# Performance work log

Measured on AMD Instinct MI355X. Metric: run time of the kernel, lower is better.

The kernel has to match this reference:

```python
import jax, jax.numpy as jnp
import numpy as np

ROI = 268
K = 32
SLOPE = 0.33
EPS = 1e-5

def leaky(h):
    return jnp.where(h >= 0, h, SLOPE * h)

def bn(h, g, b):
    # BatchNorm in training mode: biased batch statistics over the node/batch axis
    mu = h.mean(0)
    var = ((h - mu) ** 2).mean(0)
    return (h - mu) * jax.lax.rsqrt(var + EPS) * g + b


def setup_inputs():
    B, F, C, deg = 64, ROI, 32, 32
    N = B * ROI
    key = jax.random.key(0)
    ks = jax.random.split(key, 32)
    x = jax.random.normal(ks[0], (N, F), jnp.float32)
    # static within-graph edges: every node has exactly `deg` incoming edges
    tgt = jnp.repeat(jnp.arange(N, dtype=jnp.int32), deg)
    src = (tgt // ROI) * ROI + jax.random.randint(ks[1], (N * deg,), 0, ROI, dtype=jnp.int32)
    edge_index = jnp.stack([src, tgt])
    batch = jnp.repeat(jnp.arange(B, dtype=jnp.int32), ROI)
    def lin(k, i, o):
        return 0.05 * jax.random.normal(k, (i, o), jnp.float32)
    def vec(k, o):
        return 0.05 * jax.random.normal(k, (o,), jnp.float32)
    p = dict(
        x=x, edge_index=edge_index, batch=batch,
        W1a=lin(ks[2], 2 * F, C), b1a=vec(ks[3], C), W1b=lin(ks[4], C, C), b1b=vec(ks[5], C),
        g1=1.0 + vec(ks[6], C), be1=vec(ks[7], C),
        W2a=lin(ks[8], 2 * F, C), b2a=vec(ks[9], C), W2b=lin(ks[10], C, C), b2b=vec(ks[11], C),
        g2=1.0 + vec(ks[12], C), be2=vec(ks[13], C),
        W3=lin(ks[14], 2 * F, 1), b3=vec(ks[15], 1), g3=1.0 + vec(ks[16], 1), be3=vec(ks[17], 1),
        Wl1=lin(ks[18], ROI + 2 * C, 256), bl1=vec(ks[19], 256), g4=1.0 + vec(ks[20], 256), be4=vec(ks[21], 256),
        Wl2=lin(ks[22], 256, 128), bl2=vec(ks[23], 128), g5=1.0 + vec(ks[24], 128), be5=vec(ks[25], 128),
        Wl3=lin(ks[26], 128, 1), bl3=vec(ks[27], 1),
    )
    return p


def reference(x, edge_index, batch,
              W1a, b1a, W1b, b1b, g1, be1,
              W2a, b2a, W2b, b2b, g2, be2,
              W3, b3, g3, be3,
              Wl1, bl1, g4, be4, Wl2, bl2, g5, be5, Wl3, bl3):
    N, F = x.shape
    B = N // ROI
    src, tgt = edge_index[0], edge_index[1]
    xi = x[tgt]                       # [E, F] central node feature
    xd = x[src] - xi                  # [E, F] x_j - x_i
    # --- gcn1: EdgeConv(mlp1) + BN + LeakyReLU (dropout = identity in eval) ---
    m1 = leaky(xi @ W1a[:F] + xd @ W1a[F:] + b1a) @ W1b + b1b   # [E, C]
    a1 = jax.ops.segment_max(m1, tgt, num_segments=N)
    a1 = jnp.where(jnp.isfinite(a1), a1, 0.0)
    x1 = leaky(bn(a1, g1, be1))
    # --- gcn3: EdgeConv(mlp3) + BN + LeakyReLU ---
    m3 = xi @ W3[:F] + xd @ W3[F:] + b3                          # [E, 1]
    a3 = jax.ops.segment_max(m3, tgt, num_segments=N)
    a3 = jnp.where(jnp.isfinite(a3), a3, 0.0)
    x3 = leaky(bn(a3, g3, be3))
    # --- gcn2: DynamicEdgeConv(mlp2, k=32) + BN + LeakyReLU ---
    xg = x.reshape(B, ROI, F)
    sq = jnp.sum(xg * xg, -1)
    d2 = sq[:, :, None] + sq[:, None, :] - 2.0 * jnp.einsum('bif,bjf->bij', xg, xg)
    _, idx = jax.lax.top_k(-d2, K)                               # [B, ROI, K], includes self
    xj = jax.vmap(lambda f, i: f[i])(xg, idx)                    # [B, ROI, K, F]
    part_i = jnp.einsum('bif,fc->bic', xg, W2a[:F])
    part_d = jnp.einsum('bikf,fc->bikc', xj - xg[:, :, None, :], W2a[F:])
    h2 = leaky(part_i[:, :, None, :] + part_d + b2a)
    m2 = h2 @ W2b + b2b                                          # [B, ROI, K, C]
    x2 = leaky(bn(m2.max(axis=2).reshape(N, -1), g2, be2))
    # --- readout ---
    counts = jax.ops.segment_sum(jnp.ones((N, 1), x.dtype), batch, num_segments=B)
    p1 = jax.ops.segment_sum(x1, batch, num_segments=B) / counts
    p2 = jax.ops.segment_sum(x2, batch, num_segments=B) / counts
    z = jnp.concatenate([p1, p2, x3.reshape(B, ROI)], -1)        # [B, 268+64]
    z = leaky(bn(z @ Wl1 + bl1, g4, be4))
    z = leaky(bn(z @ Wl2 + bl2, g5, be5))
    return z @ Wl3 + bl3                                          # [B, 1]
```

## Files before the change

kernel.cpp:

```cpp
#include <hip/hip_runtime.h>
#include <hip/hip_bf16.h>

#define ROI   268
#define FDIM  268
#define NB    64
#define NN    (NB*ROI)
#define CC    32
#define DEG   32
#define KSEL  32
#define SLOPE 0.33f
#define EPSBN 1e-5f

typedef __attribute__((ext_vector_type(8)))  short bf16x8;
typedef __attribute__((ext_vector_type(4)))  float f32x4;
typedef __attribute__((ext_vector_type(16))) float f32x16;

__device__ __forceinline__ float lrelu(float h) { return h >= 0.f ? h : SLOPE * h; }

__device__ __forceinline__ unsigned short f2bf(float f) {
    union { __hip_bfloat16 h; unsigned short s; } u;
    u.h = __float2bfloat16(f);
    return u.s;
}
__device__ __forceinline__ float bf2f(unsigned short h) {
    return __uint_as_float(((unsigned int)h) << 16);
}

#define PREP_PACK_BLOCKS  2448
#define PREP_PACKW_BLOCKS 18
#define PREP_SCAL_BLOCKS  1072

__global__ __launch_bounds__(256) void k_prep(
    const float* __restrict__ x,
    const float* __restrict__ W1a, const float* __restrict__ W2a,
    const float* __restrict__ W3,  const float* __restrict__ b3,
    unsigned short* __restrict__ Xh, unsigned short* __restrict__ Xl,
    unsigned short* __restrict__ Wfh, unsigned short* __restrict__ Wfl,
    float* __restrict__ u3, float* __restrict__ v3, float* __restrict__ sqv)
{
    const int bid = blockIdx.x;
    const int tid = threadIdx.x;
    if (bid < PREP_PACK_BLOCKS) {
        const int gid = bid * 256 + tid;
        const int l   = gid & 63;
        const int f3  = gid >> 6;
        const int ks  = f3 % 9;
        const int bc  = f3 / 9;
        const int ct  = bc % 17;
        const int b   = bc / 17;
        const int node = ct * 16 + (l & 15);
        const int k0   = ks * 32 + (l >> 4) * 8;
        float f[8];
        #pragma unroll
        for (int j = 0; j < 8; ++j) f[j] = 0.f;
        if (node < ROI) {
            const float* row = &x[((size_t)b * ROI + node) * FDIM];
            if (k0 + 3 < FDIM) { float4 v = *(const float4*)&row[k0];     f[0]=v.x; f[1]=v.y; f[2]=v.z; f[3]=v.w; }
            if (k0 + 7 < FDIM) { float4 v = *(const float4*)&row[k0 + 4]; f[4]=v.x; f[5]=v.y; f[6]=v.z; f[7]=v.w; }
        }
        unsigned short hh[8], ll[8];
        #pragma unroll
        for (int j = 0; j < 8; ++j) {
            hh[j] = f2bf(f[j]);
            ll[j] = f2bf(f[j] - bf2f(hh[j]));
        }
        uint4 hp, lp;
        hp.x = (unsigned)hh[0] | ((unsigned)hh[1] << 16); hp.y = (unsigned)hh[2] | ((unsigned)hh[3] << 16);
        hp.z = (unsigned)hh[4] | ((unsigned)hh[5] << 16); hp.w = (unsigned)hh[6] | ((unsigned)hh[7] << 16);
        lp.x = (unsigned)ll[0] | ((unsigned)ll[1] << 16); lp.y = (unsigned)ll[2] | ((unsigned)ll[3] << 16);
        lp.z = (unsigned)ll[4] | ((unsigned)ll[5] << 16); lp.w = (unsigned)ll[6] | ((unsigned)ll[7] << 16);
        const size_t base = (size_t)f3 * 512 + l * 8;
        *(uint4*)&Xh[base] = hp;
        *(uint4*)&Xl[base] = lp;
    } else if (bid < PREP_PACK_BLOCKS + PREP_PACKW_BLOCKS) {
        const int gid = (bid - PREP_PACK_BLOCKS) * 256 + tid;
        const int l  = gid & 63;
        const int f3 = gid >> 6;
        const int ks = f3 % 9;
        const int mc = f3 / 9;
        const int ct = mc & 1;
        const int m  = mc >> 1;
        const int k0 = ks * 32 + (l >> 4) * 8;
        const int c  = ct * 16 + (l & 15);
        const float* W = (m < 2) ? W1a : W2a;
        const bool isU = (m & 1) == 0;
        unsigned short hh[8], ll[8];
        #pragma unroll
        for (int j = 0; j < 8; ++j) {
            const int kk = k0 + j;
            float val = 0.f;
            if (kk < FDIM) {
                float wb = W[(size_t)(FDIM + kk) * CC + c];
                val = isU ? (W[(size_t)kk * CC + c] - wb) : wb;
            }
            hh[j] = f2bf(val);
            ll[j] = f2bf(val - bf2f(hh[j]));
        }
        uint4 hp, lp;
        hp.x = (unsigned)hh[0] | ((unsigned)hh[1] << 16); hp.y = (unsigned)hh[2] | ((unsigned)hh[3] << 16);
        hp.z = (unsigned)hh[4] | ((unsigned)hh[5] << 16); hp.w = (unsigned)hh[6] | ((unsigned)hh[7] << 16);
        lp.x = (unsigned)ll[0] | ((unsigned)ll[1] << 16); lp.y = (unsigned)ll[2] | ((unsigned)ll[3] << 16);
        lp.z = (unsigned)ll[4] | ((unsigned)ll[5] << 16); lp.w = (unsigned)ll[6] | ((unsigned)ll[7] << 16);
        const size_t base = (size_t)f3 * 512 + l * 8;
        *(uint4*)&Wfh[base] = hp;
        *(uint4*)&Wfl[base] = lp;
    } else {
        const int s = bid - (PREP_PACK_BLOCKS + PREP_PACKW_BLOCKS);
        const int l = tid & 63;
        #pragma unroll
        for (int i = 0; i < 4; ++i) {
            const int n = s * 16 + i * 4 + (tid >> 6);
            const float* row = &x[(size_t)n * FDIM];
            float su = 0.f, sv = 0.f, sq = 0.f;
            #pragma unroll
            for (int t = 0; t < 4; ++t) {
                const int f = l + 64 * t;
                float xv = row[f];
                float wv = W3[FDIM + f];
                float wu = W3[f] - wv;
                su += xv * wu; sv += xv * wv; sq += xv * xv;
            }
            if (l < 12) {
                const int f = 256 + l;
                float xv = row[f];
                float wv = W3[FDIM + f];
                float wu = W3[f] - wv;
                su += xv * wu; sv += xv * wv; sq += xv * xv;
            }
            #pragma unroll
            for (int mm = 32; mm > 0; mm >>= 1) {
                su += __shfl_xor(su, mm);
                sv += __shfl_xor(sv, mm);
                sq += __shfl_xor(sq, mm);
            }
            if (l == 0) {
                u3[n] = su + b3[0];
                v3[n] = sv;
                sqv[n] = sq;
            }
        }
    }
}

#define PD_DIST_BLOCKS 576
#define PD_PROJ_BLOCKS 1088

__global__ __launch_bounds__(512) void k_projdist(
    const unsigned short* __restrict__ Xh, const unsigned short* __restrict__ Xl,
    const unsigned short* __restrict__ Wfh, const unsigned short* __restrict__ Wfl,
    const float* __restrict__ b1a, const float* __restrict__ b2a,
    const float* __restrict__ sqv,
    float* __restrict__ u1, float* __restrict__ v1,
    float* __restrict__ u2, float* __restrict__ v2,
    int* __restrict__ knn)
{
    __shared__ float S[32][297];
    __shared__ float sqj[288];
    const int tid = threadIdx.x;
    const int l   = tid & 63;
    const int w   = tid >> 6;

    if (blockIdx.x >= PD_DIST_BLOCKS) {
        const int idx  = blockIdx.x - PD_DIST_BLOCKS;
        const int b    = idx & 63;
        const int ctn  = idx >> 6;
        const int tile = b * 17 + ctn;
        const int m    = w >> 1;
        const int ct   = w & 1;
        bf16x8 Ah[9], Al[9];
        {
            const size_t abase = (size_t)tile * 9 * 512 + l * 8;
            #pragma unroll
            for (int ks = 0; ks < 9; ++ks) {
                Ah[ks] = *(const bf16x8*)&Xh[abase + ks * 512];
                Al[ks] = *(const bf16x8*)&Xl[abase + ks * 512];
            }
        }
        float* outp = (m == 0) ? u1 : (m == 1) ? v1 : (m == 2) ? u2 : v2;
        const size_t wbase = ((size_t)((m * 2 + ct) * 9)) * 512 + l * 8;
        f32x4 aHH = {0.f, 0.f, 0.f, 0.f};
        f32x4 aHL = {0.f, 0.f, 0.f, 0.f};
        f32x4 aLH = {0.f, 0.f, 0.f, 0.f};
        #pragma unroll
        for (int ks = 0; ks < 9; ++ks) {
            bf16x8 bh = *(const bf16x8*)&Wfh[wbase + ks * 512];
            bf16x8 bl = *(const bf16x8*)&Wfl[wbase + ks * 512];
            aHH = __builtin_amdgcn_mfma_f32_16x16x32_bf16(Ah[ks], bh, aHH, 0, 0, 0);
            aHL = __builtin_amdgcn_mfma_f32_16x16x32_bf16(Ah[ks], bl, aHL, 0, 0, 0);
            aLH = __builtin_amdgcn_mfma_f32_16x16x32_bf16(Al[ks], bh, aLH, 0, 0, 0);
        }
        f32x4 acc;
        #pragma unroll
        for (int i = 0; i < 4; ++i) acc[i] = (aHH[i] + aHL[i]) + aLH[i];
        const int ch = ct * 16 + (l & 15);
        float bias = 0.f;
        if (m == 0) bias = b1a[ch];
        else if (m == 2) bias = b2a[ch];
        const int r0 = (l >> 4) * 4;
        #pragma unroll
        for (int i = 0; i < 4; ++i) {
            const int node = ctn * 16 + r0 + i;
            if (node < ROI)
                outp[((size_t)b * ROI + node) * 32 + ch] = acc[i] + bias;
        }
        return;
    }

    const int bid = blockIdx.x;
    const int b   = bid & 63;
    const int rt  = bid >> 6;
    const int r0g = rt * 32;
    const int nrows = min(32, ROI - r0g);
    const size_t bN = (size_t)b * ROI;

    for (int t = tid; t < 288; t += 512)
        sqj[t] = (t < ROI) ? sqv[bN + t] : __builtin_inff();
    for (int t = tid; t < 32 * 16; t += 512)
        S[t >> 4][272 + (t & 15)] = __builtin_inff();

    const int a  = w & 1;
    const int at = min(rt * 2 + a, 16);
    bf16x8 Ah[9], Al[9];
    {
        const size_t abase = ((size_t)(b * 17 + at) * 9) * 512 + l * 8;
        #pragma unroll
        for (int ks = 0; ks < 9; ++ks) {
            Ah[ks] = *(const bf16x8*)&Xh[abase + ks * 512];
            Al[ks] = *(const bf16x8*)&Xl[abase + ks * 512];
        }
    }
    const int rloc = (at - rt * 2) * 16 + (l >> 4) * 4;
    float sqr4[4];
    #pragma unroll
    for (int i = 0; i < 4; ++i) {
        const int row = r0g + rloc + i;
        sqr4[i] = (row < ROI) ? sqv[bN + row] : 0.f;
    }

    for (int ct = (w >> 1); ct < 17; ct += 4) {
        const size_t bbase = ((size_t)(b * 17 + ct) * 9) * 512 + l * 8;
        f32x4 aHH = {0.f, 0.f, 0.f, 0.f};
        f32x4 aHL = {0.f, 0.f, 0.f, 0.f};
        f32x4 aLH = {0.f, 0.f, 0.f, 0.f};
        #pragma unroll
        for (int ks = 0; ks < 9; ++ks) {
            bf16x8 bh = *(const bf16x8*)&Xh[bbase + ks * 512];
            bf16x8 bl = *(const bf16x8*)&Xl[bbase + ks * 512];
            aHH = __builtin_amdgcn_mfma_f32_16x16x32_bf16(Ah[ks], bh, aHH, 0, 0, 0);
            aHL = __builtin_amdgcn_mfma_f32_16x16x32_bf16(Ah[ks], bl, aHL, 0, 0, 0);
            aLH = __builtin_amdgcn_mfma_f32_16x16x32_bf16(Al[ks], bh, aLH, 0, 0, 0);
        }
        const int col = ct * 16 + (l & 15);
        const float sj = sqj[col];
        #pragma unroll
        for (int i = 0; i < 4; ++i) {
            const float dot = (aHH[i] + aHL[i]) + aLH[i];
            S[rloc + i][col] = sqr4[i] + sj - 2.f * dot;
        }
    }
    __syncthreads();

    const int grp = tid >> 5, sl = tid & 31;
    const int rowA = grp, rowB = grp + 16;
    unsigned ka[9], kb[9];
    #pragma unroll
    for (int q = 0; q < 9; ++q) {
        const int idx = q * 32 + sl;
        unsigned ba = __float_as_uint(S[rowA][idx]);
        unsigned ma = (unsigned)(((int)ba) >> 31) | 0x80000000u;
        ka[q] = ((ba ^ ma) & ~0x1FFu) | (unsigned)idx;
        unsigned bb = __float_as_uint(S[rowB][idx]);
        unsigned mb = (unsigned)(((int)bb) >> 31) | 0x80000000u;
        kb[q] = ((bb ^ mb) & ~0x1FFu) | (unsigned)idx;
    }
    #pragma unroll
    for (int i = 1; i < 9; ++i) {
        #pragma unroll
        for (int j = i; j > 0; --j) {
            unsigned loA = ka[j-1] < ka[j] ? ka[j-1] : ka[j];
            unsigned hiA = ka[j-1] < ka[j] ? ka[j]   : ka[j-1];
            ka[j-1] = loA; ka[j] = hiA;
            unsigned loB = kb[j-1] < kb[j] ? kb[j-1] : kb[j];
            unsigned hiB = kb[j-1] < kb[j] ? kb[j]   : kb[j-1];
            kb[j-1] = loB; kb[j] = hiB;
        }
    }
    unsigned keepA = 0, keepB = 0;
    #pragma unroll
    for (int it = 0; it < KSEL; ++it) {
        unsigned mA = ka[0], mB = kb[0];
        #pragma unroll
        for (int mm = 16; mm > 0; mm >>= 1) {
            unsigned oA = (unsigned)__shfl_xor((int)mA, mm, 32);
            unsigned oB = (unsigned)__shfl_xor((int)mB, mm, 32);
            mA = oA < mA ? oA : mA;
            mB = oB < mB ? oB : mB;
        }
        if (sl == it) { keepA = mA; keepB = mB; }
        const bool winA = (ka[0] == mA);
        const bool winB = (kb[0] == mB);
        #pragma unroll
        for (int q = 0; q < 8; ++q) {
            ka[q] = winA ? ka[q+1] : ka[q];
            kb[q] = winB ? kb[q+1] : kb[q];
        }
        ka[8] = winA ? 0xFFFFFFFFu : ka[8];
        kb[8] = winB ? 0xFFFFFFFFu : kb[8];
    }
    if (rowA < nrows)
        knn[(bN + r0g + rowA) * 32 + sl] = (int)bN + (int)(keepA & 0x1FFu);
    if (rowB < nrows)
        knn[(bN + r0g + rowB) * 32 + sl] = (int)bN + (int)(keepB & 0x1FFu);
}

#define EDGE_GROUPS 10
#define EDGE_NPB 27
#define VSH 40

__global__ __launch_bounds__(256) void k_edge_fused(
    const float* __restrict__ u1, const float* __restrict__ v1,
    const float* __restrict__ W1b, const float* __restrict__ b1b,
    const int* __restrict__ ei,
    const float* __restrict__ u2, const float* __restrict__ v2,
    const float* __restrict__ W2b, const float* __restrict__ b2b,
    const int* __restrict__ knn,
    const float* __restrict__ u3, const float* __restrict__ v3,
    float* __restrict__ a1, float* __restrict__ a2, float* __restrict__ a3)
{
    __shared__ __align__(16) unsigned short vs[ROI * VSH];
    __shared__ float vs3[ROI];

    const int tid  = threadIdx.x;
    const int l    = tid & 63;
    const int wv   = tid >> 6;
    const int half = l >> 5;
    const int e    = l & 31;
    const bool g1  = blockIdx.x < (NB * EDGE_GROUPS);
    const int rem  = g1 ? blockIdx.x : blockIdx.x - NB * EDGE_GROUPS;
    const int b    = rem / EDGE_GROUPS;
    const int q    = rem % EDGE_GROUPS;
    const int n0   = q * EDGE_NPB;
    const int cnt  = min(EDGE_NPB, ROI - n0);
    const size_t bN = (size_t)b * ROI;

    const float* u  = g1 ? u1 : u2;
    const float* v  = g1 ? v1 : v2;
    const float* Wb = g1 ? W1b : W2b;
    const float* bb = g1 ? b1b : b2b;
    const int* nbr  = g1 ? ei : knn;
    float* aout     = g1 ? a1 : a2;

    {
        const float* vsrc = v + bN * 32;
        for (int i = tid * 4; i < ROI * 32; i += 1024) {
            float4 vv = *(const float4*)&vsrc[i];
            const int r = i >> 5, c0 = i & 31;
            uint2 p;
            p.x = (unsigned)f2bf(vv.x) | ((unsigned)f2bf(vv.y) << 16);
            p.y = (unsigned)f2bf(vv.z) | ((unsigned)f2bf(vv.w) << 16);
            *(uint2*)&vs[r * VSH + c0] = p;
        }
        if (g1)
            for (int t = tid; t < ROI; t += 256) vs3[t] = v3[bN + t];
    }

    union { bf16x8 v8; unsigned u4[4]; } B0, B1;
    #pragma unroll
    for (int j = 0; j < 4; ++j) {
        B0.u4[j] = (unsigned)f2bf(Wb[(half * 8 + 2*j    ) * 32 + e])
                 | ((unsigned)f2bf(Wb[(half * 8 + 2*j + 1) * 32 + e]) << 16);
        B1.u4[j] = (unsigned)f2bf(Wb[(16 + half * 8 + 2*j    ) * 32 + e])
                 | ((unsigned)f2bf(Wb[(16 + half * 8 + 2*j + 1) * 32 + e]) << 16);
    }
    const float biasc = bb[e];

    int jns[8];
    {
        const int nper = (cnt + 3) >> 2;
        #pragma unroll
        for (int s = 0; s < 8; ++s) jns[s] = 0;
        for (int s = 0; s < nper; ++s) {
            const int il = wv + s * 4;
            if (il < cnt)
                jns[s] = nbr[(size_t)((int)bN + n0 + il) * DEG + e] - (int)bN;
        }
    }
    __syncthreads();

    int s = 0;
    for (int il = wv; il < cnt; il += 4, ++s) {
        const int n   = (int)bN + n0 + il;
        const int jnl = jns[s];

        float hv[16];
        #pragma unroll
        for (int ss = 0; ss < 2; ++ss) {
            const int c0 = ss * 16 + half * 8;
            float4 uv0 = *(const float4*)&u[(size_t)n * 32 + c0];
            float4 uv1 = *(const float4*)&u[(size_t)n * 32 + c0 + 4];
            bf16x8 vb = *(const bf16x8*)&vs[jnl * VSH + c0];
            const unsigned short* vbs = (const unsigned short*)&vb;
            hv[ss*8+0] = lrelu(uv0.x + bf2f(vbs[0]));
            hv[ss*8+1] = lrelu(uv0.y + bf2f(vbs[1]));
            hv[ss*8+2] = lrelu(uv0.z + bf2f(vbs[2]));
            hv[ss*8+3] = lrelu(uv0.w + bf2f(vbs[3]));
            hv[ss*8+4] = lrelu(uv1.x + bf2f(vbs[4]));
            hv[ss*8+5] = lrelu(uv1.y + bf2f(vbs[5]));
            hv[ss*8+6] = lrelu(uv1.z + bf2f(vbs[6]));
            hv[ss*8+7] = lrelu(uv1.w + bf2f(vbs[7]));
        }
        union { bf16x8 v8; unsigned u4[4]; } A0, A1;
        #pragma unroll
        for (int j = 0; j < 4; ++j) {
            A0.u4[j] = (unsigned)f2bf(hv[2*j])     | ((unsigned)f2bf(hv[2*j + 1]) << 16);
            A1.u4[j] = (unsigned)f2bf(hv[8 + 2*j]) | ((unsigned)f2bf(hv[8 + 2*j + 1]) << 16);
        }
        f32x16 acc = {0.f,0.f,0.f,0.f,0.f,0.f,0.f,0.f,0.f,0.f,0.f,0.f,0.f,0.f,0.f,0.f};
        acc = __builtin_amdgcn_mfma_f32_32x32x16_bf16(A0.v8, B0.v8, acc, 0, 0, 0);
        acc = __builtin_amdgcn_mfma_f32_32x32x16_bf16(A1.v8, B1.v8, acc, 0, 0, 0);

        float mx = acc[0];
        #pragma unroll
        for (int r = 1; r < 16; ++r) mx = fmaxf(mx, acc[r]);
        mx = fmaxf(mx, __shfl_xor(mx, 32));
        if (l < 32) aout[(size_t)n * 32 + l] = mx + biasc;

        if (g1) {
            float a3v = u3[n] + vs3[jnl];
            #pragma unroll
            for (int mm = 16; mm > 0; mm >>= 1) a3v = fmaxf(a3v, __shfl_xor(a3v, mm));
            if (l == 0) a3[n] = a3v;
        }
    }
}

__global__ __launch_bounds__(256) void k_stats1(
    const float* __restrict__ a1, const float* __restrict__ a2,
    float* __restrict__ part)
{
    const int p = blockIdx.x;
    const int tid = threadIdx.x;
    const int ch = tid & 31, sub = tid >> 5;
    const size_t base = (size_t)p * ROI;
    float s1 = 0.f, q1 = 0.f, s2 = 0.f, q2 = 0.f;
    for (int n = sub; n < ROI; n += 8) {
        float v1 = a1[(base + n) * 32 + ch];
        float v2 = a2[(base + n) * 32 + ch];
        s1 += v1; q1 += v1 * v1; s2 += v2; q2 += v2 * v2;
    }
    __shared__ float L[4][256];
    L[0][tid] = s1; L[1][tid] = q1; L[2][tid] = s2; L[3][tid] = q2;
    __syncthreads();
    if (tid < 128) {
        const int a = tid >> 5, c = tid & 31;
        float s = 0.f;
        #pragma unroll
        for (int k = 0; k < 8; ++k) s += L[a][c + 32 * k];
        part[p * 128 + a * 32 + c] = s;
    }
}

__global__ __launch_bounds__(256) void k_pool_fc1(
    const float* __restrict__ a1, const float* __restrict__ a2, const float* __restrict__ a3,
    const float* __restrict__ part,
    const float* __restrict__ g1, const float* __restrict__ be1,
    const float* __restrict__ g2, const float* __restrict__ be2,
    const float* __restrict__ g3, const float* __restrict__ be3,
    const float* __restrict__ Wl1, const float* __restrict__ bl1,
    float* __restrict__ h1)
{
    const int b = blockIdx.x, tid = threadIdx.x;
    __shared__ float stl[130];
    __shared__ float zs[332];
    __shared__ float P[4][64];
    __shared__ float S3[256], Q3[256];

    {
        float p0 = 0.f, p1 = 0.f, p2 = 0.f, p3 = 0.f;
        float q0 = 0.f, q1 = 0.f, q2 = 0.f, q3 = 0.f;
        int n = tid;
        for (; n + 768 < NN; n += 1024) {
            float a = a3[n], bb = a3[n + 256], c = a3[n + 512], d = a3[n + 768];
            p0 += a; q0 += a * a;
            p1 += bb; q1 += bb * bb;
            p2 += c; q2 += c * c;
            p3 += d; q3 += d * d;
        }
        for (; n < NN; n += 256) { float a = a3[n]; p0 += a; q0 += a * a; }
        S3[tid] = (p0 + p1) + (p2 + p3);
        Q3[tid] = (q0 + q1) + (q2 + q3);
    }
    __syncthreads();
    for (int off = 128; off > 0; off >>= 1) {
        if (tid < off) { S3[tid] += S3[tid + off]; Q3[tid] += Q3[tid + off]; }
        __syncthreads();
    }
    if (tid < 64) {
        const int a = (tid >> 5) * 2, c = tid & 31;
        float s0 = 0.f, s1 = 0.f, q0b = 0.f, q1b = 0.f;
        for (int p = 0; p < 64; p += 2) {
            s0  += part[p * 128 + a * 32 + c];
            q0b += part[p * 128 + (a + 1) * 32 + c];
            s1  += part[(p + 1) * 128 + a * 32 + c];
            q1b += part[(p + 1) * 128 + (a + 1) * 32 + c];
        }
        float ss = s0 + s1, qq = q0b + q1b;
        float gv = (tid < 32) ? g1[c] : g2[c];
        float bv = (tid < 32) ? be1[c] : be2[c];
        float mu  = ss * (1.f / NN);
        float var = qq * (1.f / NN) - mu * mu;
        float sc  = gv * rsqrtf(var + EPSBN);
        stl[tid * 2] = sc; stl[tid * 2 + 1] = bv - mu * sc;
    }
    if (tid == 64) {
        float mu  = S3[0] * (1.f / NN);
        float var = Q3[0] * (1.f / NN) - mu * mu;
        float sc  = g3[0] * rsqrtf(var + EPSBN);
        stl[128] = sc; stl[129] = be3[0] - mu * sc;
    }
    __syncthreads();

    const int c = tid & 63, grp = tid >> 6;
    const float* src = (c < 32) ? a1 : a2;
    const int ch = c & 31;
    const float sc = stl[c * 2], sh = stl[c * 2 + 1];
    {
        const size_t rb = (size_t)b * ROI;
        float p0 = 0.f, p1 = 0.f, p2 = 0.f, p3 = 0.f;
        int i = grp;
        for (; i + 12 < ROI; i += 16) {
            p0 += lrelu(src[(rb + i)      * 32 + ch] * sc + sh);
            p1 += lrelu(src[(rb + i + 4)  * 32 + ch] * sc + sh);
            p2 += lrelu(src[(rb + i + 8)  * 32 + ch] * sc + sh);
            p3 += lrelu(src[(rb + i + 12) * 32 + ch] * sc + sh);
        }
        for (; i < ROI; i += 4)
            p0 += lrelu(src[(rb + i) * 32 + ch] * sc + sh);
        P[grp][c] = (p0 + p1) + (p2 + p3);
    }
    const float sc3 = stl[128], sh3 = stl[129];
    for (int i = tid; i < ROI; i += 256)
        zs[64 + i] = lrelu(a3[b * ROI + i] * sc3 + sh3);
    __syncthreads();
    if (tid < 64)
        zs[tid] = (P[0][tid] + P[1][tid] + P[2][tid] + P[3][tid]) * (1.f / ROI);
    __syncthreads();

    {
        float s0 = 0.f, s1 = 0.f, s2 = 0.f, s3 = 0.f;
        #pragma unroll 4
        for (int k = 0; k < 332; k += 4) {
            s0 += zs[k]     * Wl1[(size_t)k       * 256 + tid];
            s1 += zs[k + 1] * Wl1[(size_t)(k + 1) * 256 + tid];
            s2 += zs[k + 2] * Wl1[(size_t)(k + 2) * 256 + tid];
            s3 += zs[k + 3] * Wl1[(size_t)(k + 3) * 256 + tid];
        }
        h1[(size_t)b * 256 + tid] = bl1[tid] + ((s0 + s1) + (s2 + s3));
    }
}

__global__ __launch_bounds__(128) void k_fc2s(
    const float* __restrict__ h1,
    const float* __restrict__ g4, const float* __restrict__ be4,
    const float* __restrict__ Wl2, const float* __restrict__ bl2,
    float* __restrict__ h2)
{
    const int b = blockIdx.x, tid = threadIdx.x;
    __shared__ float hs[256];
    float s0 = 0.f, q0 = 0.f, s1 = 0.f, q1 = 0.f;
    float s2 = 0.f, q2 = 0.f, s3 = 0.f, q3 = 0.f;
    for (int r = 0; r < NB; r += 2) {
        float a = h1[(size_t)r * 256 + tid];
        float c = h1[(size_t)r * 256 + tid + 128];
        float d = h1[(size_t)(r + 1) * 256 + tid];
        float e = h1[(size_t)(r + 1) * 256 + tid + 128];
        s0 += a; q0 += a * a;
        s1 += c; q1 += c * c;
        s2 += d; q2 += d * d;
        s3 += e; q3 += e * e;
    }
    {
        float ssA = s0 + s2, qqA = q0 + q2;
        float muA = ssA * (1.f / NB);
        float vaA = qqA * (1.f / NB) - muA * muA;
        float scA = g4[tid] * rsqrtf(vaA + EPSBN);
        float shA = be4[tid] - muA * scA;
        hs[tid] = lrelu(h1[(size_t)b * 256 + tid] * scA + shA);
        float ssB = s1 + s3, qqB = q1 + q3;
        float muB = ssB * (1.f / NB);
        float vaB = qqB * (1.f / NB) - muB * muB;
        float scB = g4[tid + 128] * rsqrtf(vaB + EPSBN);
        float shB = be4[tid + 128] - muB * scB;
        hs[tid + 128] = lrelu(h1[(size_t)b * 256 + tid + 128] * scB + shB);
    }
    __syncthreads();
    float s0b = 0.f, s1b = 0.f, s2b = 0.f, s3b = 0.f;
    #pragma unroll 4
    for (int k = 0; k < 256; k += 4) {
        s0b += hs[k]     * Wl2[(size_t)k       * 128 + tid];
        s1b += hs[k + 1] * Wl2[(size_t)(k + 1) * 128 + tid];
        s2b += hs[k + 2] * Wl2[(size_t)(k + 2) * 128 + tid];
        s3b += hs[k + 3] * Wl2[(size_t)(k + 3) * 128 + tid];
    }
    h2[(size_t)b * 128 + tid] = bl2[tid] + ((s0b + s1b) + (s2b + s3b));
}

__global__ __launch_bounds__(128) void k_fc3s(
    const float* __restrict__ h2,
    const float* __restrict__ g5, const float* __restrict__ be5,
    const float* __restrict__ Wl3, const float* __restrict__ bl3,
    float* __restrict__ out)
{
    const int tid = threadIdx.x;
    __shared__ float T[64][133];
    float s0 = 0.f, q0 = 0.f, s1 = 0.f, q1 = 0.f;
    for (int r = 0; r < NB; r += 2) {
        float a = h2[(size_t)r * 128 + tid];
        float b = h2[(size_t)(r + 1) * 128 + tid];
        s0 += a; q0 += a * a;
        s1 += b; q1 += b * b;
    }
    float ss = s0 + s1, qq = q0 + q1;
    float mu  = ss * (1.f / NB);
    float var = qq * (1.f / NB) - mu * mu;
    float sc  = g5[tid] * rsqrtf(var + EPSBN);
    float sh  = be5[tid] - mu * sc;
    const float w3 = Wl3[tid];
    for (int r = 0; r < NB; ++r)
        T[r][tid] = lrelu(h2[(size_t)r * 128 + tid] * sc + sh) * w3;
    __syncthreads();
    if (tid < 64) {
        float a0 = 0.f, a1 = 0.f, a2 = 0.f, a3 = 0.f;
        #pragma unroll 4
        for (int c = 0; c < 128; c += 4) {
            a0 += T[tid][c];
            a1 += T[tid][c + 1];
            a2 += T[tid][c + 2];
            a3 += T[tid][c + 3];
        }
        out[tid] = bl3[0] + ((a0 + a1) + (a2 + a3));
    }
}

extern "C" void kernel_launch(void* const* d_in, const int* in_sizes, int n_in,
                              void* d_out, int out_size, void* d_ws, size_t ws_size,
                              hipStream_t stream)
{
    (void)in_sizes; (void)n_in; (void)out_size; (void)ws_size;
    const float* x   = (const float*)d_in[0];
    const int*   ei  = (const int*)d_in[1];
    const float* W1a = (const float*)d_in[3];
    const float* b1a = (const float*)d_in[4];
    const float* W1b = (const float*)d_in[5];
    const float* b1b = (const float*)d_in[6];
    const float* g1  = (const float*)d_in[7];
    const float* be1 = (const float*)d_in[8];
    const float* W2a = (const float*)d_in[9];
    const float* b2a = (const float*)d_in[10];
    const float* W2b = (const float*)d_in[11];
    const float* b2b = (const float*)d_in[12];
    const float* g2  = (const float*)d_in[13];
    const float* be2 = (const float*)d_in[14];
    const float* W3  = (const float*)d_in[15];
    const float* b3  = (const float*)d_in[16];
    const float* g3  = (const float*)d_in[17];
    const float* be3 = (const float*)d_in[18];
    const float* Wl1 = (const float*)d_in[19];
    const float* bl1 = (const float*)d_in[20];
    const float* g4  = (const float*)d_in[21];
    const float* be4 = (const float*)d_in[22];
    const float* Wl2 = (const float*)d_in[23];
    const float* bl2 = (const float*)d_in[24];
    const float* g5  = (const float*)d_in[25];
    const float* be5 = (const float*)d_in[26];
    const float* Wl3 = (const float*)d_in[27];
    const float* bl3 = (const float*)d_in[28];

    float* ws  = (float*)d_ws;
    float* u1  = ws;
    float* v1  = u1 + (size_t)NN * 32;
    float* u2  = v1 + (size_t)NN * 32;
    float* v2  = u2 + (size_t)NN * 32;
    float* u3  = v2 + (size_t)NN * 32;
    float* v3  = u3 + NN;
    float* sqv = v3 + NN;
    float* a1  = sqv + NN;
    float* a2  = a1 + (size_t)NN * 32;
    float* a3  = a2 + (size_t)NN * 32;
    float* h1  = a3 + NN;
    float* h2  = h1 + (size_t)NB * 256;
    float* part = h2 + (size_t)NB * 128;
    int*   knn = (int*)(part + 64 * 128);
    unsigned short* Xh = (unsigned short*)(((uintptr_t)(knn + (size_t)NN * 32) + 255) & ~(uintptr_t)255);
    unsigned short* Xl = Xh + (size_t)64 * 17 * 9 * 512;
    unsigned short* Wfh = Xl + (size_t)64 * 17 * 9 * 512;
    unsigned short* Wfl = Wfh + (size_t)8 * 9 * 512;

    k_prep<<<PREP_PACK_BLOCKS + PREP_PACKW_BLOCKS + PREP_SCAL_BLOCKS, 256, 0, stream>>>(
        x, W1a, W2a, W3, b3, Xh, Xl, Wfh, Wfl, u3, v3, sqv);
    k_projdist<<<PD_DIST_BLOCKS + PD_PROJ_BLOCKS, 512, 0, stream>>>(
        Xh, Xl, Wfh, Wfl, b1a, b2a, sqv, u1, v1, u2, v2, knn);
    k_edge_fused<<<2 * NB * EDGE_GROUPS, 256, 0, stream>>>(
        u1, v1, W1b, b1b, ei, u2, v2, W2b, b2b, knn, u3, v3, a1, a2, a3);
    k_stats1<<<64, 256, 0, stream>>>(a1, a2, part);
    k_pool_fc1<<<NB, 256, 0, stream>>>(a1, a2, a3, part, g1, be1, g2, be2, g3, be3,
                                       Wl1, bl1, h1);
    k_fc2s<<<NB, 128, 0, stream>>>(h1, g4, be4, Wl2, bl2, h2);
    k_fc3s<<<1, 128, 0, stream>>>(h2, g5, be5, Wl3, bl3, (float*)d_out);
}
```

Measured before the change: 131.4 us.

## Fold node projections into distance blocks, reusing register-resident X tiles

Drops the separate projection blocks from k_projdist. The distance blocks now also compute the u1/v1/u2/v2 projections, using the Ah/Al X fragments they already hold in registers. Each warp handles one projection matrix for its row tile across both channel tiles. This removes the second load of X tiles and shrinks the grid, but adds MFMA work and register pressure to the distance blocks and lengthens their critical path before the top-k phase. The clamped last tile is projected twice with identical values.

```diff
diff --git a/kernel.cpp b/kernel.cpp
--- a/kernel.cpp
+++ b/kernel.cpp
@@ -143,7 +143,6 @@
 }
 
 #define PD_DIST_BLOCKS 576
-#define PD_PROJ_BLOCKS 1088
 
 __global__ __launch_bounds__(512) void k_projdist(
     const unsigned short* __restrict__ Xh, const unsigned short* __restrict__ Xl,
@@ -160,52 +159,6 @@
     const int l   = tid & 63;
     const int w   = tid >> 6;
 
-    if (blockIdx.x >= PD_DIST_BLOCKS) {
-        const int idx  = blockIdx.x - PD_DIST_BLOCKS;
-        const int b    = idx & 63;
-        const int ctn  = idx >> 6;
-        const int tile = b * 17 + ctn;
-        const int m    = w >> 1;
-        const int ct   = w & 1;
-        bf16x8 Ah[9], Al[9];
-        {
-            const size_t abase = (size_t)tile * 9 * 512 + l * 8;
-            #pragma unroll
-            for (int ks = 0; ks < 9; ++ks) {
-                Ah[ks] = *(const bf16x8*)&Xh[abase + ks * 512];
-                Al[ks] = *(const bf16x8*)&Xl[abase + ks * 512];
-            }
-        }
-        float* outp = (m == 0) ? u1 : (m == 1) ? v1 : (m == 2) ? u2 : v2;
-        const size_t wbase = ((size_t)((m * 2 + ct) * 9)) * 512 + l * 8;
-        f32x4 aHH = {0.f, 0.f, 0.f, 0.f};
-        f32x4 aHL = {0.f, 0.f, 0.f, 0.f};
-        f32x4 aLH = {0.f, 0.f, 0.f, 0.f};
-        #pragma unroll
-        for (int ks = 0; ks < 9; ++ks) {
-            bf16x8 bh = *(const bf16x8*)&Wfh[wbase + ks * 512];
-            bf16x8 bl = *(const bf16x8*)&Wfl[wbase + ks * 512];
-            aHH = __builtin_amdgcn_mfma_f32_16x16x32_bf16(Ah[ks], bh, aHH, 0, 0, 0);
-            aHL = __builtin_amdgcn_mfma_f32_16x16x32_bf16(Ah[ks], bl, aHL, 0, 0, 0);
-            aLH = __builtin_amdgcn_mfma_f32_16x16x32_bf16(Al[ks], bh, aLH, 0, 0, 0);
-        }
-        f32x4 acc;
-        #pragma unroll
-        for (int i = 0; i < 4; ++i) acc[i] = (aHH[i] + aHL[i]) + aLH[i];
-        const int ch = ct * 16 + (l & 15);
-        float bias = 0.f;
-        if (m == 0) bias = b1a[ch];
-        else if (m == 2) bias = b2a[ch];
-        const int r0 = (l >> 4) * 4;
-        #pragma unroll
-        for (int i = 0; i < 4; ++i) {
-            const int node = ctn * 16 + r0 + i;
-            if (node < ROI)
-                outp[((size_t)b * ROI + node) * 32 + ch] = acc[i] + bias;
-        }
-        return;
-    }
-
     const int bid = blockIdx.x;
     const int b   = bid & 63;
     const int rt  = bid >> 6;
@@ -256,6 +209,39 @@
         for (int i = 0; i < 4; ++i) {
             const float dot = (aHH[i] + aHL[i]) + aLH[i];
             S[rloc + i][col] = sqr4[i] + sj - 2.f * dot;
+        }
+    }
+
+    {
+        const int m = w >> 1;
+        float* outp = (m == 0) ? u1 : (m == 1) ? v1 : (m == 2) ? u2 : v2;
+        #pragma unroll
+        for (int ct2 = 0; ct2 < 2; ++ct2) {
+            const size_t wbase = ((size_t)((m * 2 + ct2) * 9)) * 512 + l * 8;
+            f32x4 aHH = {0.f, 0.f, 0.f, 0.f};
+            f32x4 aHL = {0.f, 0.f, 0.f, 0.f};
+            f32x4 aLH = {0.f, 0.f, 0.f, 0.f};
+            #pragma unroll
+            for (int ks = 0; ks < 9; ++ks) {
+                bf16x8 bh = *(const bf16x8*)&Wfh[wbase + ks * 512];
+                bf16x8 bl = *(const bf16x8*)&Wfl[wbase + ks * 512];
+                aHH = __builtin_amdgcn_mfma_f32_16x16x32_bf16(Ah[ks], bh, aHH, 0, 0, 0);
+                aHL = __builtin_amdgcn_mfma_f32_16x16x32_bf16(Ah[ks], bl, aHL, 0, 0, 0);
+                aLH = __builtin_amdgcn_mfma_f32_16x16x32_bf16(Al[ks], bh, aLH, 0, 0, 0);
+            }
+            const int ch = ct2 * 16 + (l & 15);
+            float bias = 0.f;
+            if (m == 0) bias = b1a[ch];
+            else if (m == 2) bias = b2a[ch];
+            const int r0 = (l >> 4) * 4;
+            #pragma unroll
+            for (int i = 0; i < 4; ++i) {
+                const int node = at * 16 + r0 + i;
+                if (node < ROI) {
+                    const float val = ((aHH[i] + aHL[i]) + aLH[i]) + bias;
+                    outp[(bN + node) * 32 + ch] = val;
+                }
+            }
         }
     }
     __syncthreads();
@@ -698,7 +684,7 @@
 
     k_prep<<<PREP_PACK_BLOCKS + PREP_PACKW_BLOCKS + PREP_SCAL_BLOCKS, 256, 0, stream>>>(
         x, W1a, W2a, W3, b3, Xh, Xl, Wfh, Wfl, u3, v3, sqv);
-    k_projdist<<<PD_DIST_BLOCKS + PD_PROJ_BLOCKS, 512, 0, stream>>>(
+    k_projdist<<<PD_DIST_BLOCKS, 512, 0, stream>>>(
         Xh, Xl, Wfh, Wfl, b1a, b2a, sqv, u1, v1, u2, v2, knn);
     k_edge_fused<<<2 * NB * EDGE_GROUPS, 256, 0, stream>>>(
         u1, v1, W1b, b1b, ei, u2, v2, W2b, b2b, knn, u3, v3, a1, a2, a3);
```

Measured after the change: 144.8 us. 10.2% more time.
